# Optimization experiments

Hardware: AMD Instinct MI355X
Metric: run time of the kernel (lower is better)

## Reference

```python
import jax, jax.numpy as jnp
import numpy as np
from jax import lax

B, C, H, W = 64, 384, 28, 28
E, K, R = 3, 2, 8          # num_experts, top_k, lora rank
HID = 4 * C                # ConvNeXt MLP hidden
EPS = 1e-6
SCALING = 8.0 / 8.0        # alpha / r


def setup_inputs() -> dict:
    key = jax.random.key(0)
    ks = jax.random.split(key, 18)
    N = B * H * W
    f32 = jnp.float32
    inp = {
        "x": jax.random.normal(ks[0], (B, C, H, W), f32),
        "conv_w": jax.random.normal(ks[1], (C, 1, 7, 7), f32) * 0.05,
        "conv_b": jax.random.normal(ks[2], (C,), f32) * 0.02,
        "norm_g": 1.0 + jax.random.normal(ks[3], (C,), f32) * 0.02,
        "norm_b": jax.random.normal(ks[4], (C,), f32) * 0.02,
        "dom_g": jax.random.normal(ks[5], (E, C), f32) * 0.02,
        "dom_b": jax.random.normal(ks[6], (E, C), f32) * 0.02,
        "fc1_w": jax.random.normal(ks[7], (C, HID), f32) * (C ** -0.5),
        "fc1_b": jax.random.normal(ks[8], (HID,), f32) * 0.02,
        "fc2_w": jax.random.normal(ks[9], (HID, C), f32) * (HID ** -0.5),
        "fc2_b": jax.random.normal(ks[10], (C,), f32) * 0.02,
        "w_down": jax.random.normal(ks[11], (E, C, R), f32) * (C ** -0.5),
        "w_up": jax.random.normal(ks[12], (E, R, C), f32) * 0.02,
        "gamma": jax.random.normal(ks[13], (C,), f32) * 0.1,
        "routing_weights": jax.nn.softmax(jax.random.normal(ks[14], (B, E), f32), axis=-1),
        "topk_probs": jax.nn.softmax(jax.random.normal(ks[15], (N, K), f32), axis=-1),
        "topk_indices": jax.random.randint(ks[16], (N, K), 0, E),
    }
    return inp


def _forward(x, conv_w, conv_b, norm_g, norm_b, dom_g, dom_b,
             fc1_w, fc1_b, fc2_w, fc2_b, w_down, w_up, gamma,
             routing_weights, topk_probs, topk_indices):
    shortcut = x
    # depthwise 7x7 conv, NCHW, SAME padding
    y = lax.conv_general_dilated(
        x, conv_w, window_strides=(1, 1), padding=((3, 3), (3, 3)),
        feature_group_count=C,
        dimension_numbers=("NCHW", "OIHW", "NCHW"))
    y = y + conv_b[None, :, None, None]
    y = jnp.transpose(y, (0, 2, 3, 1))  # [B, H, W, C] channels-last path

    # ParallelMoELayerNorm: orig LN + sum_i w_i * LN_i(x). All LNs share eps,
    # so normalize once and fuse affine params per-sample.
    mu = jnp.mean(y, axis=-1, keepdims=True)
    var = jnp.mean(jnp.square(y - mu), axis=-1, keepdims=True)
    xhat = (y - mu) * lax.rsqrt(var + EPS)
    g_eff = norm_g[None, :] + routing_weights @ dom_g   # [B, C]
    b_eff = norm_b[None, :] + routing_weights @ dom_b   # [B, C]
    y = xhat * g_eff[:, None, None, :] + b_eff[:, None, None, :]

    # base ConvNeXt MLP (exact GELU, as torch nn.GELU)
    h = jax.nn.gelu(jnp.einsum("bhwc,cf->bhwf", y, fc1_w) + fc1_b,
                    approximate=False)
    orig_out = jnp.einsum("bhwf,fc->bhwc", h, fc2_w) + fc2_b

    # MoE LoRA: dense per-expert rank-8 compute, combined with top-k weights.
    # Equivalent math to the gather/matmul/scatter-add loop in the source.
    y_flat = y.reshape(-1, C)                                   # [N, C]
    down = jnp.einsum("nc,ecr->enr", y_flat, w_down)            # [E, N, R]
    up = jnp.einsum("enr,erc->enc", jax.nn.gelu(down, approximate=False), w_up)
    # combine weights: comb[n, e] = sum_k topk_probs[n, k] * (topk_indices[n,k]==e)
    comb = jnp.sum(jax.nn.one_hot(topk_indices, E, dtype=y.dtype)
                   * topk_probs[..., None], axis=1)             # [N, E]
    moe_out = jnp.einsum("enc,ne->nc", up * SCALING, comb)
    y = orig_out + moe_out.reshape(B, H, W, C)

    y = jnp.transpose(y, (0, 3, 1, 2))  # back to NCHW
    y = gamma[None, :, None, None] * y  # layer scale; drop_path = identity (eval)
    return y + shortcut


def reference(x, conv_w, conv_b, norm_g, norm_b, dom_g, dom_b,
              fc1_w, fc1_b, fc2_w, fc2_b, w_down, w_up, gamma,
              routing_weights, topk_probs, topk_indices):
    return _forward(x, conv_w, conv_b, norm_g, norm_b, dom_g, dom_b,
                    fc1_w, fc1_b, fc2_w, fc2_b, w_down, w_up, gamma,
                    routing_weights, topk_probs, topk_indices)
```

## Files before the change

### kernel.cpp

```cpp
#include <hip/hip_runtime.h>
#include <hip/hip_bf16.h>
#include <cstdint>
#include <cstddef>

constexpr int cB   = 64;
constexpr int cC   = 384;
constexpr int cH   = 28;
constexpr int cW   = 28;
constexpr int cHID = 1536;
constexpr int cNTOK = cB * cH * cW;
constexpr int cKP   = cHID + 32;
constexpr int cCH   = 2;
constexpr int cMR   = cNTOK / cCH;

typedef __attribute__((ext_vector_type(8))) short bf16x8;
typedef __attribute__((ext_vector_type(4))) float f32x4;

__device__ __forceinline__ float gelu_f(float x) {
  float u = 1.5957691216057308f * x * (1.0f + 0.044715f * x * x);
  float e = __expf(-u);
  return x / (1.0f + e);
}

__device__ __forceinline__ float bf16_to_f(short s) {
  return __uint_as_float(((unsigned)(unsigned short)s) << 16);
}

__device__ __forceinline__ void gload_lds16(const void* g, void* l) {
  __builtin_amdgcn_global_load_lds(
      (const __attribute__((address_space(1))) unsigned int*)g,
      (__attribute__((address_space(3))) unsigned int*)l, 16, 0, 0);
}

__global__ __launch_bounds__(256) void prep_eff(
    const float* __restrict__ ng, const float* __restrict__ nb,
    const float* __restrict__ dg, const float* __restrict__ db,
    const float* __restrict__ rw, float* __restrict__ geff, float* __restrict__ beff) {
  int i = blockIdx.x * 256 + threadIdx.x;
  if (i >= cB * cC) return;
  int b = i / cC, c = i - b * cC;
  float g = ng[c], bb = nb[c];
#pragma unroll
  for (int e = 0; e < 3; ++e) {
    float r = rw[b * 3 + e];
    g += r * dg[e * cC + c];
    bb += r * db[e * cC + c];
  }
  geff[i] = g;
  beff[i] = bb;
}

__global__ __launch_bounds__(256) void transpose_bf16(
    const float* __restrict__ w, __hip_bfloat16* __restrict__ wt, int R0, int C0) {
  __shared__ float t[64][65];
  int c0 = blockIdx.x * 64, r0 = blockIdx.y * 64;
  for (int i = threadIdx.x; i < 64 * 64; i += 256) {
    int r = i >> 6, c = i & 63;
    t[r][c] = w[(size_t)(r0 + r) * C0 + c0 + c];
  }
  __syncthreads();
  for (int i = threadIdx.x; i < 64 * 64; i += 256) {
    int c = i >> 6, r = i & 63;
    wt[(size_t)(c0 + c) * R0 + r0 + r] = __float2bfloat16(t[r][c]);
  }
}

__global__ __launch_bounds__(256) void build_fc2t(
    const float* __restrict__ fc2w, const float* __restrict__ wu,
    __hip_bfloat16* __restrict__ fc2t) {
  int i = blockIdx.x * 256 + threadIdx.x;
  if (i >= cC * cKP) return;
  int c = i / cKP, k = i - c * cKP;
  float v = 0.f;
  if (k < cHID) v = fc2w[(size_t)k * cC + c];
  else {
    int j = k - cHID;
    if (j < 24) v = wu[(size_t)(j >> 3) * 8 * cC + (size_t)(j & 7) * cC + c];
  }
  fc2t[i] = __float2bfloat16(v);
}

__global__ __launch_bounds__(256) void build_wdt(
    const float* __restrict__ wd, __hip_bfloat16* __restrict__ wdt) {
  int i = blockIdx.x * 256 + threadIdx.x;
  if (i >= 32 * cC) return;
  int j = i / cC, c = i - j * cC;
  float v = 0.f;
  if (j < 24) v = wd[(size_t)(j >> 3) * cC * 8 + (size_t)c * 8 + (j & 7)];
  wdt[i] = __float2bfloat16(v);
}

constexpr int cPL = 8;
__global__ __launch_bounds__(256) void conv_dw(
    const float* __restrict__ x, const float* __restrict__ cw,
    const float* __restrict__ cb, float* __restrict__ out) {
  int pb = blockIdx.x * cPL;
  int c0 = pb % cC;
  __shared__ __align__(16) float tile[cPL][34][36];
  __shared__ float wsm[cPL][49];
  const int tid = threadIdx.x;

  float4 z4 = {0.f, 0.f, 0.f, 0.f};
  for (int i = tid; i < cPL * 34 * 9; i += 256)
    ((float4*)tile)[i] = z4;
  __syncthreads();

  for (int i = tid; i < cPL * 196; i += 256) {
    int p = i / 196, q = i - p * 196;
    int r = q / 7, cl = (q - r * 7) * 4;
    float4 v = *(const float4*)&x[(size_t)(pb + p) * 784 + r * 28 + cl];
    *(float4*)&tile[p][r + 3][cl + 4] = v;
  }
  for (int i = tid; i < cPL * 49; i += 256) {
    int p = i / 49, k = i - p * 49;
    wsm[p][k] = cw[(size_t)(c0 + p) * 49 + k];
  }
  __syncthreads();

  if (tid < cPL * 28) {
    int p = tid / 28, r = tid - p * 28;
    float acc[28];
    float cbv = cb[c0 + p];
#pragma unroll
    for (int w = 0; w < 28; ++w) acc[w] = cbv;
    for (int dh = 0; dh < 7; ++dh) {
      float rowv[36];
      const float4* rp = (const float4*)&tile[p][r + dh][0];
#pragma unroll
      for (int k = 0; k < 9; ++k) ((float4*)rowv)[k] = rp[k];
      float w7[7];
#pragma unroll
      for (int dw = 0; dw < 7; ++dw) w7[dw] = wsm[p][dh * 7 + dw];
#pragma unroll
      for (int w = 0; w < 28; ++w)
#pragma unroll
        for (int dw = 0; dw < 7; ++dw)
          acc[w] += rowv[w + dw + 1] * w7[dw];
    }
    float* op = out + (size_t)(pb + p) * 784 + r * 28;
#pragma unroll
    for (int k = 0; k < 7; ++k)
      *(float4*)&op[k * 4] = *(float4*)&acc[k * 4];
  }
}

__global__ __launch_bounds__(256) void ln_affine(
    const float* __restrict__ convout, const float* __restrict__ geff,
    const float* __restrict__ beff, __hip_bfloat16* __restrict__ y) {
  int bh = blockIdx.x;
  int b = bh / cH;
  int hrow = bh - b * cH;
  __shared__ float t[cC * 29];
  const float* src = convout + (size_t)b * cC * (cH * cW) + (size_t)hrow * cW;
  for (int i = threadIdx.x; i < cC * cW; i += 256) {
    int c = i / cW, w = i - c * cW;
    t[c * 29 + w] = src[(size_t)c * (cH * cW) + w];
  }
  __syncthreads();
  int wave = threadIdx.x >> 6, lane = threadIdx.x & 63;
  const float* gp = geff + (size_t)b * cC;
  const float* bp = beff + (size_t)b * cC;
  for (int w = wave; w < cW; w += 4) {
    float v[6], s = 0.f, s2 = 0.f;
#pragma unroll
    for (int j = 0; j < 6; ++j) {
      v[j] = t[(lane + 64 * j) * 29 + w];
      s += v[j];
      s2 += v[j] * v[j];
    }
#pragma unroll
    for (int d = 32; d; d >>= 1) {
      s += __shfl_xor(s, d);
      s2 += __shfl_xor(s2, d);
    }
    float mu = s * (1.0f / cC);
    float var = s2 * (1.0f / cC) - mu * mu;
    float rstd = rsqrtf(var + 1e-6f);
    size_t n = (size_t)bh * cW + w;
#pragma unroll
    for (int j = 0; j < 6; ++j) {
      int c = lane + 64 * j;
      float val = (v[j] - mu) * rstd * gp[c] + bp[c];
      y[n * cC + c] = __float2bfloat16(val);
    }
  }
}

template <int DO_GELU>
__global__ __launch_bounds__(256) void gemm_bt(
    const __hip_bfloat16* __restrict__ A, int lda,
    const __hip_bfloat16* __restrict__ Bt,
    const float* __restrict__ bias,
    __hip_bfloat16* __restrict__ Cb, int ldc,
    int M, int N, int K, int NT_N) {
  __shared__ __align__(16) __hip_bfloat16 As[128 * 32];
  __shared__ __align__(16) __hip_bfloat16 Bs[128 * 32];

  const int gsz = 8 * NT_N;
  const int g = blockIdx.x / gsz;
  const int q = blockIdx.x - g * gsz;
  const int mi = g * 8 + q / NT_N;
  const int ni = q - (q / NT_N) * NT_N;
  const int m0 = mi * 128, n0 = ni * 128;

  const int tid = threadIdx.x;
  const int lane = tid & 63;
  const int wid = tid >> 6;
  const int wm = wid >> 1, wn = wid & 1;

  const int base0 = wid * 2048;
  const int base1 = base0 + 1024;
  const int off0 = base0 + lane * 16, off1 = base1 + lane * 16;
  const int row0 = off0 >> 6, col0 = (off0 >> 1) & 31;
  const int row1 = off1 >> 6, col1 = (off1 >> 1) & 31;
  const __hip_bfloat16* pa0 = &A[(size_t)(m0 + row0) * lda + col0];
  const __hip_bfloat16* pa1 = &A[(size_t)(m0 + row1) * lda + col1];
  const __hip_bfloat16* pb0 = &Bt[(size_t)(n0 + row0) * K + col0];
  const __hip_bfloat16* pb1 = &Bt[(size_t)(n0 + row1) * K + col1];

  f32x4 acc[4][4] = {};

  for (int kt = 0; kt < K; kt += 32) {
    gload_lds16(pa0, (char*)As + base0);
    gload_lds16(pa1, (char*)As + base1);
    gload_lds16(pb0, (char*)Bs + base0);
    gload_lds16(pb1, (char*)Bs + base1);
    pa0 += 32; pa1 += 32; pb0 += 32; pb1 += 32;
    __syncthreads();
    bf16x8 af[4], bfr[4];
#pragma unroll
    for (int i = 0; i < 4; ++i)
      af[i] = *(const bf16x8*)&As[(wm * 64 + i * 16 + (lane & 15)) * 32 + (lane >> 4) * 8];
#pragma unroll
    for (int i = 0; i < 4; ++i)
      bfr[i] = *(const bf16x8*)&Bs[(wn * 64 + i * 16 + (lane & 15)) * 32 + (lane >> 4) * 8];
#pragma unroll
    for (int i = 0; i < 4; ++i)
#pragma unroll
      for (int j = 0; j < 4; ++j)
        acc[i][j] = __builtin_amdgcn_mfma_f32_16x16x32_bf16(af[i], bfr[j], acc[i][j], 0, 0, 0);
    __syncthreads();
  }

#pragma unroll
  for (int i = 0; i < 4; ++i) {
    int row = m0 + wm * 64 + i * 16 + (lane >> 4) * 4;
#pragma unroll
    for (int j = 0; j < 4; ++j) {
      int col = n0 + wn * 64 + j * 16 + (lane & 15);
      float bv = bias[col];
#pragma unroll
      for (int r = 0; r < 4; ++r) {
        float vv = acc[i][j][r] + bv;
        if (DO_GELU) vv = gelu_f(vv);
        Cb[(size_t)(row + r) * ldc + col] = __float2bfloat16(vv);
      }
    }
  }
}

__global__ __launch_bounds__(256) void lora_down(
    const __hip_bfloat16* __restrict__ y,
    const __hip_bfloat16* __restrict__ wdt,
    const float* __restrict__ probs,
    const int* __restrict__ inds,
    __hip_bfloat16* __restrict__ h) {
  __shared__ __align__(16) __hip_bfloat16 As[128 * 32];
  __shared__ __align__(16) __hip_bfloat16 Bsm[32 * 384];
  const int tid = threadIdx.x, lane = tid & 63, wid = tid >> 6;
  const int n0 = blockIdx.x * 128;

  for (int i = tid; i < 32 * 384 / 8; i += 256)
    ((bf16x8*)Bsm)[i] = ((const bf16x8*)wdt)[i];

  const int base0 = wid * 2048, base1 = base0 + 1024;
  const int off0 = base0 + lane * 16, off1 = base1 + lane * 16;
  const int row0 = off0 >> 6, col0 = (off0 >> 1) & 31;
  const int row1 = off1 >> 6, col1 = (off1 >> 1) & 31;
  const __hip_bfloat16* pa0 = &y[(size_t)(n0 + row0) * cC + col0];
  const __hip_bfloat16* pa1 = &y[(size_t)(n0 + row1) * cC + col1];

  f32x4 acc[2][2] = {};
  for (int kt = 0; kt < cC; kt += 32) {
    gload_lds16(pa0, (char*)As + base0);
    gload_lds16(pa1, (char*)As + base1);
    pa0 += 32; pa1 += 32;
    __syncthreads();
    bf16x8 af[2], bfr[2];
#pragma unroll
    for (int i = 0; i < 2; ++i)
      af[i] = *(const bf16x8*)&As[(wid * 32 + i * 16 + (lane & 15)) * 32 + (lane >> 4) * 8];
#pragma unroll
    for (int j = 0; j < 2; ++j)
      bfr[j] = *(const bf16x8*)&Bsm[(j * 16 + (lane & 15)) * 384 + kt + (lane >> 4) * 8];
#pragma unroll
    for (int i = 0; i < 2; ++i)
#pragma unroll
      for (int j = 0; j < 2; ++j)
        acc[i][j] = __builtin_amdgcn_mfma_f32_16x16x32_bf16(af[i], bfr[j], acc[i][j], 0, 0, 0);
    __syncthreads();
  }

#pragma unroll
  for (int i = 0; i < 2; ++i) {
#pragma unroll
    for (int j = 0; j < 2; ++j) {
      int colb = j * 16 + (lane & 15);
#pragma unroll
      for (int r = 0; r < 4; ++r) {
        int n = n0 + wid * 32 + i * 16 + (lane >> 4) * 4 + r;
        float zv = 0.f;
        if (colb < 24) {
          int e = colb >> 3;
          float comb = 0.f;
          if (inds[(size_t)n * 2] == e)     comb += probs[(size_t)n * 2];
          if (inds[(size_t)n * 2 + 1] == e) comb += probs[(size_t)n * 2 + 1];
          zv = comb * gelu_f(acc[i][j][r]);
        }
        h[(size_t)n * cKP + cHID + colb] = __float2bfloat16(zv);
      }
    }
  }
}

__global__ __launch_bounds__(256) void final_out(
    const __hip_bfloat16* __restrict__ tmp, const float* __restrict__ x,
    const float* __restrict__ gamma, float* __restrict__ out) {
  int bh = blockIdx.x;
  int b = bh / cH, hrow = bh - b * cH;
  __shared__ float t[cW * 385];
  const __hip_bfloat16* src = tmp + (size_t)bh * cW * cC;
  for (int i = threadIdx.x; i < cW * cC / 8; i += 256) {
    bf16x8 v = ((const bf16x8*)src)[i];
    int base = i * 8;
    int w = base / cC, c = base - w * cC;
#pragma unroll
    for (int k = 0; k < 8; ++k)
      t[w * 385 + c + k] = bf16_to_f(v[k]);
  }
  __syncthreads();
  const float* xb = x + (size_t)b * cC * (cH * cW) + (size_t)hrow * cW;
  float* ob = out + (size_t)b * cC * (cH * cW) + (size_t)hrow * cW;
  for (int i = threadIdx.x; i < cC * cW; i += 256) {
    int c = i / cW, w = i - c * cW;
    ob[(size_t)c * (cH * cW) + w] = gamma[c] * t[w * 385 + c] + xb[(size_t)c * (cH * cW) + w];
  }
}

extern "C" void kernel_launch(void* const* d_in, const int* in_sizes, int n_in,
                              void* d_out, int out_size, void* d_ws, size_t ws_size,
                              hipStream_t stream) {
  const float* x      = (const float*)d_in[0];
  const float* conv_w = (const float*)d_in[1];
  const float* conv_b = (const float*)d_in[2];
  const float* norm_g = (const float*)d_in[3];
  const float* norm_b = (const float*)d_in[4];
  const float* dom_g  = (const float*)d_in[5];
  const float* dom_b  = (const float*)d_in[6];
  const float* fc1_w  = (const float*)d_in[7];
  const float* fc1_b  = (const float*)d_in[8];
  const float* fc2_w  = (const float*)d_in[9];
  const float* fc2_b  = (const float*)d_in[10];
  const float* w_down = (const float*)d_in[11];
  const float* w_up   = (const float*)d_in[12];
  const float* gamma  = (const float*)d_in[13];
  const float* rw     = (const float*)d_in[14];
  const float* tkp    = (const float*)d_in[15];
  const int*   tki    = (const int*)d_in[16];
  float* out = (float*)d_out;

  char* ws = (char*)d_ws;
  __hip_bfloat16* y      = (__hip_bfloat16*)(ws + 0);
  __hip_bfloat16* tmpb   = (__hip_bfloat16*)(ws + 38535168);
  char*           hslot  = ws + 77070336;
  __hip_bfloat16* h      = (__hip_bfloat16*)hslot;
  float*          convb  = (float*)hslot;
  __hip_bfloat16* fc1t   = (__hip_bfloat16*)(ws + 155746304);
  __hip_bfloat16* fc2t   = (__hip_bfloat16*)(ws + 156925952);
  __hip_bfloat16* wdt    = (__hip_bfloat16*)(ws + 158130176);
  float*          geff   = (float*)(ws + 158154752);
  float*          beff   = (float*)(ws + 158253056);

  prep_eff<<<(cB * cC + 255) / 256, 256, 0, stream>>>(norm_g, norm_b, dom_g, dom_b, rw, geff, beff);
  transpose_bf16<<<dim3(cHID / 64, cC / 64), 256, 0, stream>>>(fc1_w, fc1t, cC, cHID);
  build_fc2t<<<(cC * cKP + 255) / 256, 256, 0, stream>>>(fc2_w, w_up, fc2t);
  build_wdt<<<(32 * cC + 255) / 256, 256, 0, stream>>>(w_down, wdt);
  conv_dw<<<cB * cC / cPL, 256, 0, stream>>>(x, conv_w, conv_b, convb);
  ln_affine<<<cB * cH, 256, 0, stream>>>(convb, geff, beff, y);

  const int NTM = cMR / 128;
  for (int ch = 0; ch < cCH; ++ch) {
    const __hip_bfloat16* ych = y + (size_t)ch * cMR * cC;
    gemm_bt<1><<<NTM * (cHID / 128), 256, 0, stream>>>(
        ych, cC, fc1t, fc1_b, h, cKP, cMR, cHID, cC, cHID / 128);
    lora_down<<<NTM, 256, 0, stream>>>(
        ych, wdt, tkp + (size_t)ch * cMR * 2, tki + (size_t)ch * cMR * 2, h);
    gemm_bt<0><<<NTM * (cC / 128), 256, 0, stream>>>(
        h, cKP, fc2t, fc2_b, tmpb + (size_t)ch * cMR * cC, cC, cMR, cC, cKP, cC / 128);
  }

  final_out<<<cB * cH, 256, 0, stream>>>(tmpb, x, gamma, out);
}
```

Measured before the change: 471.6 us.

## Double-buffer LDS tiles in GEMM and LoRA-down kernels to overlap loads

The shared-memory A/B tiles in the main bf16 GEMM and the A tile in the LoRA down-projection kernel become two ping-pong buffers. Each loop iteration now issues the async global-to-LDS load for the next K-slice before running the MFMAs on the current one. This removes the barrier that used to sit between each tile load and its use, so memory latency can hide behind compute. In exchange the GEMM's LDS footprint doubles, which may lower the number of resident blocks per CU.

```diff
diff --git a/kernel.cpp b/kernel.cpp
--- a/kernel.cpp
+++ b/kernel.cpp
@@ -193,8 +193,8 @@
     const float* __restrict__ bias,
     __hip_bfloat16* __restrict__ Cb, int ldc,
     int M, int N, int K, int NT_N) {
-  __shared__ __align__(16) __hip_bfloat16 As[128 * 32];
-  __shared__ __align__(16) __hip_bfloat16 Bs[128 * 32];
+  __shared__ __align__(16) __hip_bfloat16 As[2][128 * 32];
+  __shared__ __align__(16) __hip_bfloat16 Bs[2][128 * 32];
 
   const int gsz = 8 * NT_N;
   const int g = blockIdx.x / gsz;
@@ -218,22 +218,32 @@
   const __hip_bfloat16* pb0 = &Bt[(size_t)(n0 + row0) * K + col0];
   const __hip_bfloat16* pb1 = &Bt[(size_t)(n0 + row1) * K + col1];
 
+  const int nt = K >> 5;
+
+  gload_lds16(pa0, (char*)As[0] + base0);
+  gload_lds16(pa1, (char*)As[0] + base1);
+  gload_lds16(pb0, (char*)Bs[0] + base0);
+  gload_lds16(pb1, (char*)Bs[0] + base1);
+  pa0 += 32; pa1 += 32; pb0 += 32; pb1 += 32;
+  __syncthreads();
+
   f32x4 acc[4][4] = {};
-
-  for (int kt = 0; kt < K; kt += 32) {
-    gload_lds16(pa0, (char*)As + base0);
-    gload_lds16(pa1, (char*)As + base1);
-    gload_lds16(pb0, (char*)Bs + base0);
-    gload_lds16(pb1, (char*)Bs + base1);
-    pa0 += 32; pa1 += 32; pb0 += 32; pb1 += 32;
-    __syncthreads();
+  int cur = 0;
+  for (int t = 0; t < nt; ++t, cur ^= 1) {
+    if (t + 1 < nt) {
+      gload_lds16(pa0, (char*)As[cur ^ 1] + base0);
+      gload_lds16(pa1, (char*)As[cur ^ 1] + base1);
+      gload_lds16(pb0, (char*)Bs[cur ^ 1] + base0);
+      gload_lds16(pb1, (char*)Bs[cur ^ 1] + base1);
+      pa0 += 32; pa1 += 32; pb0 += 32; pb1 += 32;
+    }
     bf16x8 af[4], bfr[4];
 #pragma unroll
     for (int i = 0; i < 4; ++i)
-      af[i] = *(const bf16x8*)&As[(wm * 64 + i * 16 + (lane & 15)) * 32 + (lane >> 4) * 8];
+      af[i] = *(const bf16x8*)&As[cur][(wm * 64 + i * 16 + (lane & 15)) * 32 + (lane >> 4) * 8];
 #pragma unroll
     for (int i = 0; i < 4; ++i)
-      bfr[i] = *(const bf16x8*)&Bs[(wn * 64 + i * 16 + (lane & 15)) * 32 + (lane >> 4) * 8];
+      bfr[i] = *(const bf16x8*)&Bs[cur][(wn * 64 + i * 16 + (lane & 15)) * 32 + (lane >> 4) * 8];
 #pragma unroll
     for (int i = 0; i < 4; ++i)
 #pragma unroll
@@ -265,7 +275,7 @@
     const float* __restrict__ probs,
     const int* __restrict__ inds,
     __hip_bfloat16* __restrict__ h) {
-  __shared__ __align__(16) __hip_bfloat16 As[128 * 32];
+  __shared__ __align__(16) __hip_bfloat16 As[2][128 * 32];
   __shared__ __align__(16) __hip_bfloat16 Bsm[32 * 384];
   const int tid = threadIdx.x, lane = tid & 63, wid = tid >> 6;
   const int n0 = blockIdx.x * 128;
@@ -280,16 +290,25 @@
   const __hip_bfloat16* pa0 = &y[(size_t)(n0 + row0) * cC + col0];
   const __hip_bfloat16* pa1 = &y[(size_t)(n0 + row1) * cC + col1];
 
+  const int nt = cC >> 5;
+  gload_lds16(pa0, (char*)As[0] + base0);
+  gload_lds16(pa1, (char*)As[0] + base1);
+  pa0 += 32; pa1 += 32;
+  __syncthreads();
+
   f32x4 acc[2][2] = {};
-  for (int kt = 0; kt < cC; kt += 32) {
-    gload_lds16(pa0, (char*)As + base0);
-    gload_lds16(pa1, (char*)As + base1);
-    pa0 += 32; pa1 += 32;
-    __syncthreads();
+  int cur = 0;
+  for (int t = 0; t < nt; ++t, cur ^= 1) {
+    if (t + 1 < nt) {
+      gload_lds16(pa0, (char*)As[cur ^ 1] + base0);
+      gload_lds16(pa1, (char*)As[cur ^ 1] + base1);
+      pa0 += 32; pa1 += 32;
+    }
+    int kt = t * 32;
     bf16x8 af[2], bfr[2];
 #pragma unroll
     for (int i = 0; i < 2; ++i)
-      af[i] = *(const bf16x8*)&As[(wid * 32 + i * 16 + (lane & 15)) * 32 + (lane >> 4) * 8];
+      af[i] = *(const bf16x8*)&As[cur][(wid * 32 + i * 16 + (lane & 15)) * 32 + (lane >> 4) * 8];
 #pragma unroll
     for (int j = 0; j < 2; ++j)
       bfr[j] = *(const bf16x8*)&Bsm[(j * 16 + (lane & 15)) * 384 + kt + (lane >> 4) * 8];
```

Result: faster. 453.0 us (-3.9%).
